# Kernel tuning notes

Measured on AMD Instinct MI355X. Metric: run time of the kernel, lower is better.

The kernel has to match this reference:

```python
import jax, jax.numpy as jnp
import numpy as np

N_NODES = 100000
N_EDGES = 800000
IN_C, HID_C, OUT_C = 128, 64, 40


def setup_inputs() -> dict:
    key = jax.random.key(0)
    k1, k2, k3, k4, k5, k6 = jax.random.split(key, 6)
    x = jax.random.normal(k1, (N_NODES, IN_C), dtype=jnp.float32)
    edge_index = jax.random.randint(k2, (2, N_EDGES), 0, N_NODES, dtype=jnp.int64)
    W1 = jax.random.normal(k3, (IN_C, HID_C), dtype=jnp.float32) * (1.0 / np.sqrt(IN_C))
    b1 = jax.random.normal(k4, (HID_C,), dtype=jnp.float32) * 0.01
    W2 = jax.random.normal(k5, (HID_C, OUT_C), dtype=jnp.float32) * (1.0 / np.sqrt(HID_C))
    b2 = jax.random.normal(k6, (OUT_C,), dtype=jnp.float32) * 0.01
    return {"x": x, "edge_index": edge_index, "W1": W1, "b1": b1, "W2": W2, "b2": b2}


def _sg_propagate(x, src, dst, n):
    # GCN symmetric normalization (self-loops already appended by caller):
    # deg[i] = number of incoming edges at i; norm_e = deg[src]^-1/2 * deg[dst]^-1/2
    deg = jax.ops.segment_sum(jnp.ones_like(dst, dtype=x.dtype), dst, num_segments=n)
    dinv = jnp.where(deg > 0, jax.lax.rsqrt(deg), jnp.zeros_like(deg))
    norm = dinv[src] * dinv[dst]  # [E]
    # out[i] = sum_{e: dst_e=i} norm_e * x[src_e]
    return jax.ops.segment_sum(x[src] * norm[:, None], dst, num_segments=n)


def reference(x, edge_index, W1, b1, W2, b2):
    n = x.shape[0]
    loop = jnp.arange(n, dtype=edge_index.dtype)
    src = jnp.concatenate([edge_index[0], loop])
    dst = jnp.concatenate([edge_index[1], loop])
    # dropout is identity in eval mode
    h = _sg_propagate(x, src, dst, n) @ W1 + b1   # SGConv(in_c, hid_c), K=1
    h = jax.nn.relu(h)
    o = _sg_propagate(h, src, dst, n) @ W2 + b2   # SGConv(hid_c, out_c), K=1
    return jax.nn.log_softmax(o, axis=1)
```

## Files before the change

### kernel.cpp

```cpp
#include <hip/hip_runtime.h>
#include <math.h>

#define IN_C 128
#define HID_C 64
#define OUT_C 40
#define MD 64

typedef unsigned short u16;
__device__ __forceinline__ float bf2f(u16 u) {
  return __uint_as_float(((unsigned int)u) << 16);
}
__device__ __forceinline__ u16 f2bf(float f) {
  unsigned int u = __float_as_uint(f);
  u += 0x7fffu + ((u >> 16) & 1u);
  return (u16)(u >> 16);
}

__global__ void zero4_kernel(int4* __restrict__ p, long long n4) {
  long long i = (long long)blockIdx.x * blockDim.x + threadIdx.x;
  long long stride = (long long)gridDim.x * blockDim.x;
  for (; i < n4; i += stride) p[i] = make_int4(0, 0, 0, 0);
}

#define XS_LD2 36
#define DP_BLOCKS 1024
__global__ __launch_bounds__(256) void fused_dpf_gemm1_kernel(
    const int* __restrict__ eidx, int E, int* __restrict__ deg,
    int* __restrict__ csr2, const float* __restrict__ x,
    const float* __restrict__ W1, float* __restrict__ y, int n) {
  __shared__ float xs[64 * XS_LD2];
  __shared__ float wsh[32 * HID_C];
  int t = threadIdx.x;
  int b = (int)blockIdx.x;
  bool isDP;
  int bi;
  if (b < 2 * DP_BLOCKS) { isDP = (b & 1) == 0; bi = b >> 1; }
  else                   { isDP = false;        bi = b - DP_BLOCKS; }
  if (isDP) {
    int base = bi * 256 + t;
    int stride = DP_BLOCKS * 256;
    for (int e = base; e < E; e += 4 * stride) {
      int e1 = e + stride, e2 = e + 2 * stride, e3 = e + 3 * stride;
      bool g1 = e1 < E, g2 = e2 < E, g3 = e3 < E;
      int s0 = eidx[e], d0 = eidx[E + e];
      int s1 = 0, d1 = 0, s2 = 0, d2 = 0, s3 = 0, d3 = 0;
      if (g1) { s1 = eidx[e1]; d1 = eidx[E + e1]; }
      if (g2) { s2 = eidx[e2]; d2 = eidx[E + e2]; }
      if (g3) { s3 = eidx[e3]; d3 = eidx[E + e3]; }
      int p0 = atomicAdd(&deg[d0], 1);
      int p1 = g1 ? atomicAdd(&deg[d1], 1) : MD;
      int p2 = g2 ? atomicAdd(&deg[d2], 1) : MD;
      int p3 = g3 ? atomicAdd(&deg[d3], 1) : MD;
      if (p0 < MD) csr2[(size_t)d0 * MD + p0] = s0;
      if (p1 < MD) csr2[(size_t)d1 * MD + p1] = s1;
      if (p2 < MD) csr2[(size_t)d2 * MD + p2] = s2;
      if (p3 < MD) csr2[(size_t)d3 * MD + p3] = s3;
    }
    return;
  }
  int rowBase = bi * 64;
  if (rowBase >= n) return;
  const float4* xf4 = (const float4*)x;
  const float4* wf4 = (const float4*)W1;
  int tx = t & 15, ty = t >> 4;
  int i0 = ty * 4, j0 = tx * 4;
  float acc[4][4];
#pragma unroll
  for (int r = 0; r < 4; ++r)
#pragma unroll
    for (int j = 0; j < 4; ++j) acc[r][j] = 0.f;

  for (int kc = 0; kc < 4; ++kc) {
#pragma unroll
    for (int k = 0; k < 2; ++k) {
      int t4 = t + k * 256;
      int row = t4 >> 3, c4 = t4 & 7;
      int gr = rowBase + row;
      if (gr >= n) gr = n - 1;
      *(float4*)&xs[row * XS_LD2 + c4 * 4] = xf4[(size_t)gr * 32 + kc * 8 + c4];
      int wrow = t4 >> 4, wc4 = t4 & 15;
      *(float4*)&wsh[wrow * HID_C + wc4 * 4] =
          wf4[(size_t)(kc * 32 + wrow) * 16 + wc4];
    }
    __syncthreads();
#pragma unroll 2
    for (int c4 = 0; c4 < 32; c4 += 4) {
      float4 xv[4], wv[4];
#pragma unroll
      for (int r = 0; r < 4; ++r)
        xv[r] = *(const float4*)&xs[(i0 + r) * XS_LD2 + c4];
#pragma unroll
      for (int cc = 0; cc < 4; ++cc)
        wv[cc] = *(const float4*)&wsh[(c4 + cc) * HID_C + j0];
#pragma unroll
      for (int r = 0; r < 4; ++r) {
#pragma unroll
        for (int cc = 0; cc < 4; ++cc) {
          float xr = (&xv[r].x)[cc];
          acc[r][0] = fmaf(xr, wv[cc].x, acc[r][0]);
          acc[r][1] = fmaf(xr, wv[cc].y, acc[r][1]);
          acc[r][2] = fmaf(xr, wv[cc].z, acc[r][2]);
          acc[r][3] = fmaf(xr, wv[cc].w, acc[r][3]);
        }
      }
    }
    __syncthreads();
  }
#pragma unroll
  for (int r = 0; r < 4; ++r) {
    int i = rowBase + i0 + r;
    if (i < n) {
      float4 v = make_float4(acc[r][0], acc[r][1], acc[r][2], acc[r][3]);
      *(float4*)&y[(size_t)i * HID_C + j0] = v;
    }
  }
}

__global__ __launch_bounds__(256) void scale_kernel(
    const int* __restrict__ deg, const float4* __restrict__ y4,
    ushort4* __restrict__ ybf, int n) {
  long long total = (long long)n * 16;
  long long idx = (long long)blockIdx.x * blockDim.x + threadIdx.x;
  long long stride = (long long)gridDim.x * blockDim.x;
  for (; idx < total; idx += stride) {
    int i = (int)(idx >> 4);
    float di = rsqrtf((float)deg[i] + 1.0f);
    float4 v = y4[idx];
    ushort4 u;
    u.x = f2bf(di * v.x);
    u.y = f2bf(di * v.y);
    u.z = f2bf(di * v.z);
    u.w = f2bf(di * v.w);
    ybf[idx] = u;
  }
}

__global__ __launch_bounds__(256) void gather1_kernel(
    const ushort4* __restrict__ y4, const int* __restrict__ csr2,
    const int* __restrict__ deg, const float* __restrict__ b1,
    float* __restrict__ h, int n) {
  int lane = threadIdx.x & 63;
  int grp = lane >> 4;
  int q = lane & 15;
  float4 b1v = ((const float4*)b1)[q];
  int wid = (int)((blockIdx.x * blockDim.x + threadIdx.x) >> 6);
  int nw = (int)((gridDim.x * blockDim.x) >> 6);
  int ii = wid;
  int dc = 0;
  if (ii < n) dc = deg[ii];
  while (ii < n) {
    int nxt = ii + nw;
    int ndc = 0;
    if (nxt < n) ndc = deg[nxt];
    int i = __builtin_amdgcn_readfirstlane(ii);
    float di = rsqrtf((float)dc + 1.0f);
    int dcnt = dc < MD ? dc : MD;
    const int* row = csr2 + (size_t)i * MD;
    float4 acc = make_float4(0.f, 0.f, 0.f, 0.f);
    if (grp == 0) {
      ushort4 u = y4[(size_t)i * 16 + q];
      acc.x = bf2f(u.x); acc.y = bf2f(u.y); acc.z = bf2f(u.z); acc.w = bf2f(u.w);
    }
    int k = grp;
    for (; k + 4 < dcnt; k += 8) {
      int s0 = row[k], s1 = row[k + 4];
      ushort4 u0 = y4[(size_t)s0 * 16 + q];
      ushort4 u1 = y4[(size_t)s1 * 16 + q];
      acc.x += bf2f(u0.x) + bf2f(u1.x);
      acc.y += bf2f(u0.y) + bf2f(u1.y);
      acc.z += bf2f(u0.z) + bf2f(u1.z);
      acc.w += bf2f(u0.w) + bf2f(u1.w);
    }
    for (; k < dcnt; k += 4) {
      int s = row[k];
      ushort4 u = y4[(size_t)s * 16 + q];
      acc.x += bf2f(u.x); acc.y += bf2f(u.y);
      acc.z += bf2f(u.z); acc.w += bf2f(u.w);
    }
    acc.x += __shfl_xor(acc.x, 16); acc.y += __shfl_xor(acc.y, 16);
    acc.z += __shfl_xor(acc.z, 16); acc.w += __shfl_xor(acc.w, 16);
    acc.x += __shfl_xor(acc.x, 32); acc.y += __shfl_xor(acc.y, 32);
    acc.z += __shfl_xor(acc.z, 32); acc.w += __shfl_xor(acc.w, 32);
    if (grp == 0) {
      float4 hv;
      hv.x = fmaxf(fmaf(di, acc.x, b1v.x), 0.f);
      hv.y = fmaxf(fmaf(di, acc.y, b1v.y), 0.f);
      hv.z = fmaxf(fmaf(di, acc.z, b1v.z), 0.f);
      hv.w = fmaxf(fmaf(di, acc.w, b1v.w), 0.f);
      *(float4*)&h[(size_t)i * HID_C + 4 * q] = hv;
    }
    ii = nxt; dc = ndc;
  }
}

#define XS_LD 68
__global__ __launch_bounds__(256) void gemm2_kernel(
    const float* __restrict__ h, const float* __restrict__ W2,
    const int* __restrict__ deg, u16* __restrict__ z, int n) {
  __shared__ float hs[64 * XS_LD];
  __shared__ float w2s[64 * OUT_C + 32];
  int t = threadIdx.x;
  int rowBase = blockIdx.x * 64;
  const float4* hf4 = (const float4*)h;
  const float4* wf4 = (const float4*)W2;
#pragma unroll
  for (int k = 0; k < 4; ++k) {
    int t4 = t + k * 256;
    int row = t4 >> 4, c4 = t4 & 15;
    int gr = rowBase + row;
    if (gr >= n) gr = n - 1;
    *(float4*)&hs[row * XS_LD + c4 * 4] = hf4[(size_t)gr * 16 + c4];
  }
  for (int t4 = t; t4 < 640; t4 += 256)
    *(float4*)&w2s[t4 * 4] = wf4[t4];
  __syncthreads();
  int tx = t & 15, ty = t >> 4;
  int i0 = ty * 4, j0 = tx * 4;
  bool active = tx < 10;
  float acc[4][4];
#pragma unroll
  for (int r = 0; r < 4; ++r)
#pragma unroll
    for (int j = 0; j < 4; ++j) acc[r][j] = 0.f;
#pragma unroll 2
  for (int c4 = 0; c4 < 64; c4 += 4) {
    float4 hv[4], wv[4];
#pragma unroll
    for (int r = 0; r < 4; ++r)
      hv[r] = *(const float4*)&hs[(i0 + r) * XS_LD + c4];
#pragma unroll
    for (int cc = 0; cc < 4; ++cc)
      wv[cc] = *(const float4*)&w2s[(c4 + cc) * OUT_C + j0];
#pragma unroll
    for (int r = 0; r < 4; ++r) {
#pragma unroll
      for (int cc = 0; cc < 4; ++cc) {
        float hr = (&hv[r].x)[cc];
        acc[r][0] = fmaf(hr, wv[cc].x, acc[r][0]);
        acc[r][1] = fmaf(hr, wv[cc].y, acc[r][1]);
        acc[r][2] = fmaf(hr, wv[cc].z, acc[r][2]);
        acc[r][3] = fmaf(hr, wv[cc].w, acc[r][3]);
      }
    }
  }
  if (active) {
#pragma unroll
    for (int r = 0; r < 4; ++r) {
      int i = rowBase + i0 + r;
      if (i < n) {
        float d2 = rsqrtf((float)deg[i] + 1.0f);
        ushort4 u;
        u.x = f2bf(d2 * acc[r][0]);
        u.y = f2bf(d2 * acc[r][1]);
        u.z = f2bf(d2 * acc[r][2]);
        u.w = f2bf(d2 * acc[r][3]);
        *(ushort4*)&z[(size_t)i * OUT_C + j0] = u;
      }
    }
  }
}

__global__ __launch_bounds__(256) void gather40_kernel(
    const ushort4* __restrict__ z4, const int* __restrict__ csr2,
    const int* __restrict__ deg, const float* __restrict__ b2,
    float* __restrict__ out, int n) {
  int lane = threadIdx.x & 63;
  int grp = lane >> 4;
  int q = lane & 15;
  bool act = q < 10;
  float4 b2v = ((const float4*)b2)[act ? q : 0];
  int wid = (int)((blockIdx.x * blockDim.x + threadIdx.x) >> 6);
  int nw = (int)((gridDim.x * blockDim.x) >> 6);
  int ii = wid;
  int dc = 0;
  if (ii < n) dc = deg[ii];
  while (ii < n) {
    int nxt = ii + nw;
    int ndc = 0;
    if (nxt < n) ndc = deg[nxt];
    int i = __builtin_amdgcn_readfirstlane(ii);
    float di = rsqrtf((float)dc + 1.0f);
    int dcnt = dc < MD ? dc : MD;
    const int* row = csr2 + (size_t)i * MD;
    float4 acc = make_float4(0.f, 0.f, 0.f, 0.f);
    if (grp == 0 && act) {
      ushort4 u = z4[(size_t)i * 10 + q];
      acc.x = bf2f(u.x); acc.y = bf2f(u.y); acc.z = bf2f(u.z); acc.w = bf2f(u.w);
    }
    int k = grp;
    if (act) {
      for (; k + 4 < dcnt; k += 8) {
        int s0 = row[k], s1 = row[k + 4];
        ushort4 u0 = z4[(size_t)s0 * 10 + q];
        ushort4 u1 = z4[(size_t)s1 * 10 + q];
        acc.x += bf2f(u0.x) + bf2f(u1.x);
        acc.y += bf2f(u0.y) + bf2f(u1.y);
        acc.z += bf2f(u0.z) + bf2f(u1.z);
        acc.w += bf2f(u0.w) + bf2f(u1.w);
      }
      for (; k < dcnt; k += 4) {
        int s = row[k];
        ushort4 u = z4[(size_t)s * 10 + q];
        acc.x += bf2f(u.x); acc.y += bf2f(u.y);
        acc.z += bf2f(u.z); acc.w += bf2f(u.w);
      }
    }
    acc.x += __shfl_xor(acc.x, 16); acc.y += __shfl_xor(acc.y, 16);
    acc.z += __shfl_xor(acc.z, 16); acc.w += __shfl_xor(acc.w, 16);
    acc.x += __shfl_xor(acc.x, 32); acc.y += __shfl_xor(acc.y, 32);
    acc.z += __shfl_xor(acc.z, 32); acc.w += __shfl_xor(acc.w, 32);
    float4 o;
    o.x = fmaf(di, acc.x, b2v.x);
    o.y = fmaf(di, acc.y, b2v.y);
    o.z = fmaf(di, acc.z, b2v.z);
    o.w = fmaf(di, acc.w, b2v.w);
    float m = act ? fmaxf(fmaxf(o.x, o.y), fmaxf(o.z, o.w)) : -INFINITY;
    for (int off = 8; off; off >>= 1) m = fmaxf(m, __shfl_xor(m, off));
    float ex = act ? (expf(o.x - m) + expf(o.y - m) +
                      expf(o.z - m) + expf(o.w - m)) : 0.f;
    float s = ex;
    for (int off = 8; off; off >>= 1) s += __shfl_xor(s, off);
    if (lane < 16 && act) {
      float l = m + logf(s);
      float4 o2 = make_float4(o.x - l, o.y - l, o.z - l, o.w - l);
      *(float4*)&out[(size_t)i * OUT_C + 4 * q] = o2;
    }
    ii = nxt; dc = ndc;
  }
}

extern "C" void kernel_launch(void* const* d_in, const int* in_sizes, int n_in,
                              void* d_out, int out_size, void* d_ws, size_t ws_size,
                              hipStream_t stream) {
  const float* x  = (const float*)d_in[0];
  const int* eidx = (const int*)d_in[1];
  const float* W1 = (const float*)d_in[2];
  const float* b1 = (const float*)d_in[3];
  const float* W2 = (const float*)d_in[4];
  const float* b2 = (const float*)d_in[5];
  float* out = (float*)d_out;

  int n = in_sizes[0] / IN_C;
  int E = in_sizes[1] / 2;

  size_t npad = ((size_t)n + 255) & ~(size_t)255;
  size_t o_deg  = 0;
  size_t o_csr2 = o_deg + npad;
  size_t o_bufA = o_csr2 + (size_t)n * MD;
  size_t o_bufC = o_bufA + (size_t)n * HID_C;
  size_t needed = (o_bufC + (size_t)n * 32 + 64) * 4;
  if (ws_size < needed) return;

  float* ws  = (float*)d_ws;
  int* deg   = (int*)(ws + o_deg);
  int* csr2  = (int*)(ws + o_csr2);
  float* bufA = ws + o_bufA;
  float* bufC = ws + o_bufC;

  int gemmBlocks = (n + 63) / 64;

  zero4_kernel<<<128, 256, 0, stream>>>((int4*)deg, (long long)(npad / 4));
  fused_dpf_gemm1_kernel<<<DP_BLOCKS + gemmBlocks, 256, 0, stream>>>(
      eidx, E, deg, csr2, x, W1, bufA, n);

  scale_kernel<<<1024, 256, 0, stream>>>(deg, (const float4*)bufA,
                                         (ushort4*)bufC, n);

  gather1_kernel<<<2048, 256, 0, stream>>>((const ushort4*)bufC, csr2, deg,
                                           b1, bufA, n);
  gemm2_kernel<<<gemmBlocks, 256, 0, stream>>>(bufA, W2, deg, (u16*)bufC, n);
  gather40_kernel<<<2048, 256, 0, stream>>>((const ushort4*)bufC, csr2, deg,
                                            b2, out, n);
}
```

Measured before the change: 147.9 us.

## Store GEMM1 output as bf16 and pad layer-2 rows to 128 bytes

GEMM1 now writes bf16 instead of fp32, and the scale kernel rescales that buffer in place, which roughly halves the GEMM1 write and scale read traffic. The layer-2 z buffer gets a 64-element row stride instead of 40, so each gathered row starts on a 128-byte boundary. This adds one extra bf16 rounding before the degree scaling and makes the z buffer larger for the aligned gathers. Workspace buffers are reorganised to match.

```diff
diff --git a/kernel.cpp b/kernel.cpp
--- a/kernel.cpp
+++ b/kernel.cpp
@@ -5,6 +5,7 @@
 #define HID_C 64
 #define OUT_C 40
 #define MD 64
+#define ZS 64
 
 typedef unsigned short u16;
 __device__ __forceinline__ float bf2f(u16 u) {
@@ -27,7 +28,7 @@
 __global__ __launch_bounds__(256) void fused_dpf_gemm1_kernel(
     const int* __restrict__ eidx, int E, int* __restrict__ deg,
     int* __restrict__ csr2, const float* __restrict__ x,
-    const float* __restrict__ W1, float* __restrict__ y, int n) {
+    const float* __restrict__ W1, u16* __restrict__ y, int n) {
   __shared__ float xs[64 * XS_LD2];
   __shared__ float wsh[32 * HID_C];
   int t = threadIdx.x;
@@ -110,28 +111,30 @@
   for (int r = 0; r < 4; ++r) {
     int i = rowBase + i0 + r;
     if (i < n) {
-      float4 v = make_float4(acc[r][0], acc[r][1], acc[r][2], acc[r][3]);
-      *(float4*)&y[(size_t)i * HID_C + j0] = v;
+      ushort4 u;
+      u.x = f2bf(acc[r][0]);
+      u.y = f2bf(acc[r][1]);
+      u.z = f2bf(acc[r][2]);
+      u.w = f2bf(acc[r][3]);
+      *(ushort4*)&y[(size_t)i * HID_C + j0] = u;
     }
   }
 }
 
 __global__ __launch_bounds__(256) void scale_kernel(
-    const int* __restrict__ deg, const float4* __restrict__ y4,
-    ushort4* __restrict__ ybf, int n) {
+    const int* __restrict__ deg, ushort4* __restrict__ y4, int n) {
   long long total = (long long)n * 16;
   long long idx = (long long)blockIdx.x * blockDim.x + threadIdx.x;
   long long stride = (long long)gridDim.x * blockDim.x;
   for (; idx < total; idx += stride) {
     int i = (int)(idx >> 4);
     float di = rsqrtf((float)deg[i] + 1.0f);
-    float4 v = y4[idx];
-    ushort4 u;
-    u.x = f2bf(di * v.x);
-    u.y = f2bf(di * v.y);
-    u.z = f2bf(di * v.z);
-    u.w = f2bf(di * v.w);
-    ybf[idx] = u;
+    ushort4 u = y4[idx];
+    u.x = f2bf(di * bf2f(u.x));
+    u.y = f2bf(di * bf2f(u.y));
+    u.z = f2bf(di * bf2f(u.z));
+    u.w = f2bf(di * bf2f(u.w));
+    y4[idx] = u;
   }
 }
 
@@ -254,7 +257,7 @@
         u.y = f2bf(d2 * acc[r][1]);
         u.z = f2bf(d2 * acc[r][2]);
         u.w = f2bf(d2 * acc[r][3]);
-        *(ushort4*)&z[(size_t)i * OUT_C + j0] = u;
+        *(ushort4*)&z[(size_t)i * ZS + j0] = u;
       }
     }
   }
@@ -284,15 +287,15 @@
     const int* row = csr2 + (size_t)i * MD;
     float4 acc = make_float4(0.f, 0.f, 0.f, 0.f);
     if (grp == 0 && act) {
-      ushort4 u = z4[(size_t)i * 10 + q];
+      ushort4 u = z4[(size_t)i * 16 + q];
       acc.x = bf2f(u.x); acc.y = bf2f(u.y); acc.z = bf2f(u.z); acc.w = bf2f(u.w);
     }
     int k = grp;
     if (act) {
       for (; k + 4 < dcnt; k += 8) {
         int s0 = row[k], s1 = row[k + 4];
-        ushort4 u0 = z4[(size_t)s0 * 10 + q];
-        ushort4 u1 = z4[(size_t)s1 * 10 + q];
+        ushort4 u0 = z4[(size_t)s0 * 16 + q];
+        ushort4 u1 = z4[(size_t)s1 * 16 + q];
         acc.x += bf2f(u0.x) + bf2f(u1.x);
         acc.y += bf2f(u0.y) + bf2f(u1.y);
         acc.z += bf2f(u0.z) + bf2f(u1.z);
@@ -300,7 +303,7 @@
       }
       for (; k < dcnt; k += 4) {
         int s = row[k];
-        ushort4 u = z4[(size_t)s * 10 + q];
+        ushort4 u = z4[(size_t)s * 16 + q];
         acc.x += bf2f(u.x); acc.y += bf2f(u.y);
         acc.z += bf2f(u.z); acc.w += bf2f(u.w);
       }
@@ -347,15 +350,15 @@
   size_t o_deg  = 0;
   size_t o_csr2 = o_deg + npad;
   size_t o_bufA = o_csr2 + (size_t)n * MD;
-  size_t o_bufC = o_bufA + (size_t)n * HID_C;
-  size_t needed = (o_bufC + (size_t)n * 32 + 64) * 4;
+  size_t o_bufB = o_bufA + (size_t)n * 32;
+  size_t needed = (o_bufB + (size_t)n * HID_C + 64) * 4;
   if (ws_size < needed) return;
 
   float* ws  = (float*)d_ws;
   int* deg   = (int*)(ws + o_deg);
   int* csr2  = (int*)(ws + o_csr2);
-  float* bufA = ws + o_bufA;
-  float* bufC = ws + o_bufC;
+  u16* bufA  = (u16*)(ws + o_bufA);
+  float* bufB = ws + o_bufB;
 
   int gemmBlocks = (n + 63) / 64;
 
@@ -363,12 +366,11 @@
   fused_dpf_gemm1_kernel<<<DP_BLOCKS + gemmBlocks, 256, 0, stream>>>(
       eidx, E, deg, csr2, x, W1, bufA, n);
 
-  scale_kernel<<<1024, 256, 0, stream>>>(deg, (const float4*)bufA,
-                                         (ushort4*)bufC, n);
-
-  gather1_kernel<<<2048, 256, 0, stream>>>((const ushort4*)bufC, csr2, deg,
-                                           b1, bufA, n);
-  gemm2_kernel<<<gemmBlocks, 256, 0, stream>>>(bufA, W2, deg, (u16*)bufC, n);
-  gather40_kernel<<<2048, 256, 0, stream>>>((const ushort4*)bufC, csr2, deg,
+  scale_kernel<<<1024, 256, 0, stream>>>(deg, (ushort4*)bufA, n);
+
+  gather1_kernel<<<2048, 256, 0, stream>>>((const ushort4*)bufA, csr2, deg,
+                                           b1, bufB, n);
+  gemm2_kernel<<<gemmBlocks, 256, 0, stream>>>(bufB, W2, deg, (u16*)bufA, n);
+  gather40_kernel<<<2048, 256, 0, stream>>>((const ushort4*)bufA, csr2, deg,
                                             b2, out, n);
 }
```

Measured after the change: 148.4 us. Within noise of the previous version (+0.3%).
